# Performance work log

Hardware: AMD Instinct MI355X
Metric: run time of the kernel (lower is better)

Reference implementation:

```python
import jax, jax.numpy as jnp
import numpy as np

N_NODES = 200000
N_EDGES = 1600000
NUM_GRAPHS = 2000
VOCAB = 10000
D = 64
NUM_CLS = 2


def setup_inputs() -> dict:
    key = jax.random.key(0)
    ks = jax.random.split(key, 12)
    x = jax.random.randint(ks[0], (N_NODES,), 0, VOCAB, dtype=jnp.int32)
    edge_index = jax.random.randint(ks[1], (2, N_EDGES), 0, N_NODES, dtype=jnp.int32)
    edge_type = jax.random.randint(ks[2], (N_EDGES,), 0, 8, dtype=jnp.int32)
    batch = jnp.sort(jax.random.randint(ks[3], (N_NODES,), 0, NUM_GRAPHS, dtype=jnp.int32))
    embed_table = jax.random.normal(ks[4], (VOCAB, D), dtype=jnp.float32) * 0.02
    embed_table = embed_table.at[0].set(0.0)  # padding_idx=0
    W1 = jax.random.normal(ks[5], (D, D), dtype=jnp.float32) * (1.0 / np.sqrt(D))
    b1 = jnp.zeros((D,), dtype=jnp.float32)
    W2 = jax.random.normal(ks[6], (D, D), dtype=jnp.float32) * (1.0 / np.sqrt(D))
    b2 = jnp.zeros((D,), dtype=jnp.float32)
    Wlin = jax.random.normal(ks[7], (D, NUM_CLS), dtype=jnp.float32) * (1.0 / np.sqrt(D))
    blin = jnp.zeros((NUM_CLS,), dtype=jnp.float32)
    return {"x": x, "edge_index": edge_index, "edge_type": edge_type, "batch": batch,
            "embed_table": embed_table, "W1": W1, "b1": b1, "W2": W2, "b2": b2,
            "Wlin": Wlin, "blin": blin}


def reference(x, edge_index, edge_type, batch, embed_table, W1, b1, W2, b2, Wlin, blin):
    n = x.shape[0]
    # GCN normalization with self-loops (PyG GCNConv default, edge weight = 1)
    loops = jnp.arange(n, dtype=edge_index.dtype)
    src = jnp.concatenate([edge_index[0], loops])
    dst = jnp.concatenate([edge_index[1], loops])
    deg = jax.ops.segment_sum(jnp.ones_like(src, dtype=jnp.float32), dst, num_segments=n)
    dinv = jax.lax.rsqrt(deg)  # deg >= 1 due to self-loops
    norm = (dinv[src] * dinv[dst])[:, None]  # [E+N, 1]

    def gcn(h, W, b):
        h = h @ W  # transform first (small GEMM)
        agg = jax.ops.segment_sum(norm * h[src], dst, num_segments=n)
        return agg + b

    h = embed_table[x]                      # [N, D] embedding lookup
    h = jax.nn.relu(gcn(h, W1, b1))
    h = jax.nn.relu(gcn(h, W2, b2))
    # global mean pool over graphs
    sums = jax.ops.segment_sum(h, batch, num_segments=NUM_GRAPHS)
    cnts = jax.ops.segment_sum(jnp.ones((n,), dtype=h.dtype), batch, num_segments=NUM_GRAPHS)
    g = sums / jnp.maximum(cnts, 1.0)[:, None]
    return g @ Wlin + blin
```

## Files before the change

### kernel.cpp

```cpp
#include <hip/hip_runtime.h>
#include <hip/hip_fp16.h>


#define DD 64
#define BKT 256
#define MAXK 1024
#define NBLK 256
#define SLACK 772
#define BTE 1024
#define SRCMASK 0x3FFFF
#define PBUF_CAP 4096

typedef _Float16 half8_t __attribute__((ext_vector_type(8)));
typedef float float4_t __attribute__((ext_vector_type(4)));
union F4H8 { float4 f; half8_t h; };
union H8   { float4 f; __half2 h[4]; };

static __device__ __forceinline__ void atomAddF(float* p, float v) {
    unsafeAtomicAdd(p, v);
}

__global__ __launch_bounds__(BTE) void bin_count_kernel(
        const int* __restrict__ dst, int E, int CH,
        int* __restrict__ hist, int K,
        const float2* __restrict__ table2, __half2* __restrict__ th2, int n2,
        const float* __restrict__ W1, const float* __restrict__ W2,
        __half* __restrict__ w1t, __half* __restrict__ w2t) {
    __shared__ int lh[MAXK];
    int tid = threadIdx.x;
    for (int i = tid; i < K; i += BTE) lh[i] = 0;
    __syncthreads();
    int stride = gridDim.x * BTE;
    for (int i = blockIdx.x * BTE + tid; i < n2; i += stride)
        th2[i] = __float22half2_rn(table2[i]);
    for (int i = blockIdx.x * BTE + tid; i < DD * DD; i += stride) {
        int n = i >> 6, k = i & 63;
        w1t[i] = __float2half(W1[k * DD + n]);
        w2t[i] = __float2half(W2[k * DD + n]);
    }
    int e0 = blockIdx.x * CH;
    int e1 = min(E, e0 + CH);
    for (int e = e0 + tid; e < e1; e += BTE)
        atomicAdd(&lh[((unsigned)dst[e]) >> 8], 1);
    __syncthreads();
    for (int b = tid; b < K; b += BTE)
        hist[blockIdx.x * MAXK + b] = lh[b];
}

__global__ __launch_bounds__(256) void totals_kernel(
        const int* __restrict__ hist, int* __restrict__ bts,
        float* __restrict__ outacc, int K, int G2) {
    int gt = blockIdx.x * 256 + threadIdx.x;
    if (gt < G2) outacc[gt] = 0.f;
    int wid = gt >> 6;
    int lane = threadIdx.x & 63;
    if (wid >= K) return;
    const int PER = NBLK / 64;
    int s = 0;
    #pragma unroll
    for (int i = 0; i < PER; ++i)
        s += hist[(lane * PER + i) * MAXK + wid];
    #pragma unroll
    for (int off = 32; off >= 1; off >>= 1)
        s += __shfl_xor(s, off);
    if (lane == 0) bts[wid] = s;
}

__global__ __launch_bounds__(256) void scan_bb_kernel(
        const int* __restrict__ bts, int* __restrict__ bb, int K, int E) {
    __shared__ int part[256];
    int tid = threadIdx.x;
    int CH2 = (K + 255) / 256;
    int base = tid * CH2;
    int s = 0;
    for (int i = 0; i < CH2; ++i) {
        int idx = base + i;
        if (idx < K) s += bts[idx];
    }
    part[tid] = s;
    __syncthreads();
    if (tid < 64) {
        int carry = 0;
        for (int c = 0; c < 4; ++c) {
            int orig = part[c * 64 + tid];
            int v = orig;
            #pragma unroll
            for (int off = 1; off < 64; off <<= 1) {
                int t = __shfl_up(v, off);
                if (tid >= off) v += t;
            }
            int tot = __shfl(v, 63);
            part[c * 64 + tid] = v - orig + carry;
            carry += tot;
        }
    }
    __syncthreads();
    int run = part[tid];
    for (int i = 0; i < CH2; ++i) {
        int idx = base + i;
        if (idx < K) {
            bb[idx] = run;
            run += bts[idx];
        }
    }
    if (tid == 0) bb[K] = E;
}

__global__ __launch_bounds__(256) void scanB_kernel(
        const int* __restrict__ hist, const int* __restrict__ bb,
        int* __restrict__ cur, int K) {
    int wid = (blockIdx.x * 256 + threadIdx.x) >> 6;
    int lane = threadIdx.x & 63;
    if (wid >= K) return;
    int b = wid;
    const int PER = NBLK / 64;
    int v[PER];
    int sum = 0;
    #pragma unroll
    for (int i = 0; i < PER; ++i) {
        v[i] = hist[(lane * PER + i) * MAXK + b];
        sum += v[i];
    }
    int pref = sum;
    #pragma unroll
    for (int off = 1; off < 64; off <<= 1) {
        int t = __shfl_up(pref, off);
        if (lane >= off) pref += t;
    }
    int run = bb[b] + pref - sum;
    #pragma unroll
    for (int i = 0; i < PER; ++i) {
        cur[(lane * PER + i) * MAXK + b] = run;
        run += v[i];
    }
}

__global__ __launch_bounds__(BTE) void fill_kernel(
        const int* __restrict__ src, const int* __restrict__ dst, int E, int CH,
        const int* __restrict__ cur, int* __restrict__ pairbuf, int K) {
    __shared__ int lcur[MAXK];
    int tid = threadIdx.x;
    for (int b = tid; b < K; b += BTE)
        lcur[b] = cur[blockIdx.x * MAXK + b];
    __syncthreads();
    int e0 = blockIdx.x * CH;
    int e1 = min(E, e0 + CH);
    for (int e = e0 + tid; e < e1; e += BTE) {
        int s = src[e], d = dst[e];
        int pos = atomicAdd(&lcur[((unsigned)d) >> 8], 1);
        pairbuf[pos] = s | ((d & 255) << 24);
    }
}

__global__ __launch_bounds__(256) void build_csr_kernel(
        const int* __restrict__ pairbuf, const int* __restrict__ bnd,
        const int* __restrict__ x, int2* __restrict__ rowinfo,
        float2* __restrict__ xd, __half* __restrict__ dinvh,
        int* __restrict__ csr_src, __half* __restrict__ g1h, int N) {
    __shared__ int cnt[256], basel[256], curl[256];
    __shared__ int pbuf[PBUF_CAP];
    int tid = threadIdx.x;
    int b = blockIdx.x;
    int node0 = b << 8;
    cnt[tid] = 0;
    __syncthreads();
    int bb0 = bnd[b], bb1 = bnd[b + 1];
    int L = bb1 - bb0;
    bool fits = (L <= PBUF_CAP);
    if (fits) {
        for (int i = tid; i < L; i += 256) {
            int pk = pairbuf[bb0 + i];
            pbuf[i] = pk;
            atomicAdd(&cnt[((unsigned)pk) >> 24], 1);
        }
    } else {
        for (int i = bb0 + tid; i < bb1; i += 256)
            atomicAdd(&cnt[((unsigned)pairbuf[i]) >> 24], 1);
    }
    __syncthreads();
    int c  = cnt[tid];
    int pc = (c + 3) & ~3;
    {
        __syncthreads();
        basel[tid] = pc;
        __syncthreads();
        if (tid < 64) {
            int carry = 0;
            for (int cc = 0; cc < 4; ++cc) {
                int orig = basel[cc * 64 + tid];
                int v = orig;
                #pragma unroll
                for (int off = 1; off < 64; off <<= 1) {
                    int t = __shfl_up(v, off);
                    if (tid >= off) v += t;
                }
                int tot = __shfl(v, 63);
                cnt[cc * 64 + tid] = v - orig + carry;
                carry += tot;
            }
        }
        __syncthreads();
    }
    int cb0 = ((bb0 + 3) & ~3) + SLACK * b;
    int node = node0 + tid;
    int myBase = cb0 + cnt[tid];
    curl[tid] = myBase;
    if (node < N) {
        rowinfo[node] = make_int2(myBase, pc);
        float di = rsqrtf((float)c + 1.0f);
        xd[node] = make_float2(di, __int_as_float(x[node]));
        dinvh[node] = __float2half(di);
        for (int t = c; t < pc; ++t) csr_src[myBase + t] = N;
    } else if (node == N) {
        xd[N] = make_float2(0.0f, __int_as_float(0));
        dinvh[N] = __float2half(0.0f);
        float2* z = (float2*)(g1h + (size_t)N * DD);
        for (int t = 0; t < DD / 4; ++t) z[t] = make_float2(0.f, 0.f);
    }
    __syncthreads();
    if (fits) {
        for (int i = tid; i < L; i += 256) {
            int pk = pbuf[i];
            int pos = atomicAdd(&curl[((unsigned)pk) >> 24], 1);
            int s = pk & 0x00FFFFFF;
            csr_src[pos] = (int)(((unsigned)s) | (((unsigned)x[s]) << 18));
        }
    } else {
        for (int i = bb0 + tid; i < bb1; i += 256) {
            int pk = pairbuf[i];
            int pos = atomicAdd(&curl[((unsigned)pk) >> 24], 1);
            int s = pk & 0x00FFFFFF;
            csr_src[pos] = (int)(((unsigned)s) | (((unsigned)x[s]) << 18));
        }
    }
}

__global__ __launch_bounds__(256, 8) void layer1_kernel(
        const int2* __restrict__ rowinfo,
        const int* __restrict__ csr_src, const float2* __restrict__ xd,
        const __half* __restrict__ dinvh,
        const float4* __restrict__ th4, const __half* __restrict__ wt,
        const float* __restrict__ bias, __half* __restrict__ g1h, int N) {
    __shared__ float4 Hs4[32 * 9];
    __shared__ float dvs[32];
    int row0 = blockIdx.x * 32;
    int tid = threadIdx.x;
    int node_l = tid >> 3, j3 = tid & 7;
    int node = row0 + node_l;
    H8 acc0, acc1, acc2, acc3;
    acc0.f = make_float4(0.f, 0.f, 0.f, 0.f);
    acc1.f = acc0.f; acc2.f = acc0.f; acc3.f = acc0.f;
    __half2 dh = __float2half2_rn(0.f);
    if (node < N) {
        float2 sxd = xd[node];
        float di = sxd.x;
        if (j3 == 0) dvs[node_l] = di;
        dh = __float2half2_rn(di);
        H8 tv; tv.f = th4[(size_t)__float_as_int(sxd.y) * 8 + j3];
        acc0.h[0] = __hmul2(dh, tv.h[0]); acc0.h[1] = __hmul2(dh, tv.h[1]);
        acc0.h[2] = __hmul2(dh, tv.h[2]); acc0.h[3] = __hmul2(dh, tv.h[3]);
        int2 ri = rowinfo[node];
        const int4* cs = (const int4*)(csr_src + ri.x);
        int nq = ri.y >> 2;
        int q = 0;
        for (; q + 1 < nq; q += 2) {
            int4 sA = cs[q], sB = cs[q + 1];
            unsigned a0 = (unsigned)sA.x, a1 = (unsigned)sA.y;
            unsigned a2 = (unsigned)sA.z, a3 = (unsigned)sA.w;
            unsigned b0i = (unsigned)sB.x, b1i = (unsigned)sB.y;
            unsigned b2i = (unsigned)sB.z, b3i = (unsigned)sB.w;
            H8 u0, u1, u2, u3, u4, u5, u6, u7;
            u0.f = th4[(size_t)(a0 >> 18) * 8 + j3];
            u1.f = th4[(size_t)(a1 >> 18) * 8 + j3];
            u2.f = th4[(size_t)(a2 >> 18) * 8 + j3];
            u3.f = th4[(size_t)(a3 >> 18) * 8 + j3];
            u4.f = th4[(size_t)(b0i >> 18) * 8 + j3];
            u5.f = th4[(size_t)(b1i >> 18) * 8 + j3];
            u6.f = th4[(size_t)(b2i >> 18) * 8 + j3];
            u7.f = th4[(size_t)(b3i >> 18) * 8 + j3];
            __half2 w0 = __half2half2(dinvh[a0 & SRCMASK]);
            __half2 w1 = __half2half2(dinvh[a1 & SRCMASK]);
            __half2 w2 = __half2half2(dinvh[a2 & SRCMASK]);
            __half2 w3 = __half2half2(dinvh[a3 & SRCMASK]);
            __half2 w4 = __half2half2(dinvh[b0i & SRCMASK]);
            __half2 w5 = __half2half2(dinvh[b1i & SRCMASK]);
            __half2 w6 = __half2half2(dinvh[b2i & SRCMASK]);
            __half2 w7 = __half2half2(dinvh[b3i & SRCMASK]);
            #pragma unroll
            for (int t = 0; t < 4; ++t) {
                acc0.h[t] = __hfma2(w0, u0.h[t], acc0.h[t]);
                acc1.h[t] = __hfma2(w1, u1.h[t], acc1.h[t]);
                acc2.h[t] = __hfma2(w2, u2.h[t], acc2.h[t]);
                acc3.h[t] = __hfma2(w3, u3.h[t], acc3.h[t]);
                acc0.h[t] = __hfma2(w4, u4.h[t], acc0.h[t]);
                acc1.h[t] = __hfma2(w5, u5.h[t], acc1.h[t]);
                acc2.h[t] = __hfma2(w6, u6.h[t], acc2.h[t]);
                acc3.h[t] = __hfma2(w7, u7.h[t], acc3.h[t]);
            }
        }
        if (q < nq) {
            int4 sA = cs[q];
            unsigned a0 = (unsigned)sA.x, a1 = (unsigned)sA.y;
            unsigned a2 = (unsigned)sA.z, a3 = (unsigned)sA.w;
            H8 u0, u1, u2, u3;
            u0.f = th4[(size_t)(a0 >> 18) * 8 + j3];
            u1.f = th4[(size_t)(a1 >> 18) * 8 + j3];
            u2.f = th4[(size_t)(a2 >> 18) * 8 + j3];
            u3.f = th4[(size_t)(a3 >> 18) * 8 + j3];
            __half2 w0 = __half2half2(dinvh[a0 & SRCMASK]);
            __half2 w1 = __half2half2(dinvh[a1 & SRCMASK]);
            __half2 w2 = __half2half2(dinvh[a2 & SRCMASK]);
            __half2 w3 = __half2half2(dinvh[a3 & SRCMASK]);
            #pragma unroll
            for (int t = 0; t < 4; ++t) {
                acc0.h[t] = __hfma2(w0, u0.h[t], acc0.h[t]);
                acc1.h[t] = __hfma2(w1, u1.h[t], acc1.h[t]);
                acc2.h[t] = __hfma2(w2, u2.h[t], acc2.h[t]);
                acc3.h[t] = __hfma2(w3, u3.h[t], acc3.h[t]);
            }
        }
        #pragma unroll
        for (int t = 0; t < 4; ++t)
            acc0.h[t] = __hmul2(dh, __hadd2(__hadd2(acc0.h[t], acc1.h[t]),
                                            __hadd2(acc2.h[t], acc3.h[t])));
    }
    Hs4[node_l * 9 + j3] = acc0.f;
    __syncthreads();

    int wave = tid >> 6, lane = tid & 63;
    int m = lane & 15, quad = lane >> 4;
    int ncol = wave * 16 + m;
    F4H8 b0, b1;
    const float4* WT4 = (const float4*)wt;
    b0.f = WT4[ncol * 8 + quad];
    b1.f = WT4[ncol * 8 + 4 + quad];
    float bb_ = bias[ncol];
    #pragma unroll
    for (int t = 0; t < 2; ++t) {
        F4H8 a0, a1;
        a0.f = Hs4[(t * 16 + m) * 9 + quad];
        a1.f = Hs4[(t * 16 + m) * 9 + 4 + quad];
        float4_t acc = {0.f, 0.f, 0.f, 0.f};
        acc = __builtin_amdgcn_mfma_f32_16x16x32_f16(a0.h, b0.h, acc, 0, 0, 0);
        acc = __builtin_amdgcn_mfma_f32_16x16x32_f16(a1.h, b1.h, acc, 0, 0, 0);
        #pragma unroll
        for (int reg = 0; reg < 4; ++reg) {
            int row = t * 16 + quad * 4 + reg;
            int grow = row0 + row;
            if (grow < N) {
                float h = fmaxf(acc[reg] + bb_, 0.0f);
                g1h[(size_t)grow * DD + ncol] = __float2half(dvs[row] * h);
            }
        }
    }
}

__global__ __launch_bounds__(256, 8) void layer2_pool_kernel(
        const int2* __restrict__ rowinfo,
        const int* __restrict__ csr_src, const float2* __restrict__ xd,
        const float4* __restrict__ g1h4, const __half* __restrict__ wt,
        const float* __restrict__ bias, const int* __restrict__ batch,
        const float* __restrict__ Wlin, float* __restrict__ outacc, int N) {
    __shared__ float4 Hs4[32 * 9];
    __shared__ float lp0[128], lp1[128];
    __shared__ float p0s[32], p1s[32];
    __shared__ int   bat[32];
    int row0 = blockIdx.x * 32;
    int tid = threadIdx.x;
    int node_l = tid >> 3, j3 = tid & 7;
    int node = row0 + node_l;
    H8 acc0, acc1, acc2, acc3;
    acc0.f = make_float4(0.f, 0.f, 0.f, 0.f);
    acc1.f = acc0.f; acc2.f = acc0.f; acc3.f = acc0.f;
    if (node < N) {
        float di = xd[node].x;
        acc0.f = g1h4[(size_t)node * 8 + j3];
        int2 ri = rowinfo[node];
        const int4* cs = (const int4*)(csr_src + ri.x);
        int nq = ri.y >> 2;
        int q = 0;
        for (; q + 1 < nq; q += 2) {
            int4 sA = cs[q], sB = cs[q + 1];
            H8 u0, u1, u2, u3, u4, u5, u6, u7;
            u0.f = g1h4[(size_t)(sA.x & SRCMASK) * 8 + j3];
            u1.f = g1h4[(size_t)(sA.y & SRCMASK) * 8 + j3];
            u2.f = g1h4[(size_t)(sA.z & SRCMASK) * 8 + j3];
            u3.f = g1h4[(size_t)(sA.w & SRCMASK) * 8 + j3];
            u4.f = g1h4[(size_t)(sB.x & SRCMASK) * 8 + j3];
            u5.f = g1h4[(size_t)(sB.y & SRCMASK) * 8 + j3];
            u6.f = g1h4[(size_t)(sB.z & SRCMASK) * 8 + j3];
            u7.f = g1h4[(size_t)(sB.w & SRCMASK) * 8 + j3];
            #pragma unroll
            for (int t = 0; t < 4; ++t) {
                acc0.h[t] = __hadd2(acc0.h[t], u0.h[t]);
                acc1.h[t] = __hadd2(acc1.h[t], u1.h[t]);
                acc2.h[t] = __hadd2(acc2.h[t], u2.h[t]);
                acc3.h[t] = __hadd2(acc3.h[t], u3.h[t]);
                acc0.h[t] = __hadd2(acc0.h[t], u4.h[t]);
                acc1.h[t] = __hadd2(acc1.h[t], u5.h[t]);
                acc2.h[t] = __hadd2(acc2.h[t], u6.h[t]);
                acc3.h[t] = __hadd2(acc3.h[t], u7.h[t]);
            }
        }
        if (q < nq) {
            int4 sA = cs[q];
            H8 u0, u1, u2, u3;
            u0.f = g1h4[(size_t)(sA.x & SRCMASK) * 8 + j3];
            u1.f = g1h4[(size_t)(sA.y & SRCMASK) * 8 + j3];
            u2.f = g1h4[(size_t)(sA.z & SRCMASK) * 8 + j3];
            u3.f = g1h4[(size_t)(sA.w & SRCMASK) * 8 + j3];
            #pragma unroll
            for (int t = 0; t < 4; ++t) {
                acc0.h[t] = __hadd2(acc0.h[t], u0.h[t]);
                acc1.h[t] = __hadd2(acc1.h[t], u1.h[t]);
                acc2.h[t] = __hadd2(acc2.h[t], u2.h[t]);
                acc3.h[t] = __hadd2(acc3.h[t], u3.h[t]);
            }
        }
        __half2 dih = __float2half2_rn(di);
        #pragma unroll
        for (int t = 0; t < 4; ++t)
            acc0.h[t] = __hmul2(dih, __hadd2(__hadd2(acc0.h[t], acc1.h[t]),
                                             __hadd2(acc2.h[t], acc3.h[t])));
    }
    Hs4[node_l * 9 + j3] = acc0.f;
    __syncthreads();

    int wave = tid >> 6, lane = tid & 63;
    int m = lane & 15, quad = lane >> 4;
    int ncol = wave * 16 + m;
    F4H8 b0, b1;
    const float4* WT4 = (const float4*)wt;
    b0.f = WT4[ncol * 8 + quad];
    b1.f = WT4[ncol * 8 + 4 + quad];
    float bb_  = bias[ncol];
    float wl0 = Wlin[ncol * 2 + 0];
    float wl1 = Wlin[ncol * 2 + 1];
    #pragma unroll
    for (int t = 0; t < 2; ++t) {
        F4H8 a0, a1;
        a0.f = Hs4[(t * 16 + m) * 9 + quad];
        a1.f = Hs4[(t * 16 + m) * 9 + 4 + quad];
        float4_t acc = {0.f, 0.f, 0.f, 0.f};
        acc = __builtin_amdgcn_mfma_f32_16x16x32_f16(a0.h, b0.h, acc, 0, 0, 0);
        acc = __builtin_amdgcn_mfma_f32_16x16x32_f16(a1.h, b1.h, acc, 0, 0, 0);
        #pragma unroll
        for (int reg = 0; reg < 4; ++reg) {
            int row = t * 16 + quad * 4 + reg;
            int grow = row0 + row;
            float h = (grow < N) ? fmaxf(acc[reg] + bb_, 0.0f) : 0.0f;
            float p0 = h * wl0;
            float p1 = h * wl1;
            #pragma unroll
            for (int off = 8; off >= 1; off >>= 1) {
                p0 += __shfl_xor(p0, off);
                p1 += __shfl_xor(p1, off);
            }
            if (m == 0) {
                lp0[wave * 32 + row] = p0;
                lp1[wave * 32 + row] = p1;
            }
        }
    }
    __syncthreads();
    if (tid < 32) {
        int grow = row0 + tid;
        p0s[tid] = lp0[tid] + lp0[32 + tid] + lp0[64 + tid] + lp0[96 + tid];
        p1s[tid] = lp1[tid] + lp1[32 + tid] + lp1[64 + tid] + lp1[96 + tid];
        bat[tid] = (grow < N) ? batch[grow] : -1;
    }
    __syncthreads();
    if (tid < 32) {
        int bg = bat[tid];
        bool head = (bg >= 0) && (tid == 0 || bat[tid - 1] != bg);
        if (head) {
            float s0 = 0.f, s1 = 0.f;
            for (int k = tid; k < 32 && bat[k] == bg; ++k) {
                s0 += p0s[k];
                s1 += p1s[k];
            }
            atomAddF(&outacc[bg * 2 + 0], s0);
            atomAddF(&outacc[bg * 2 + 1], s1);
        }
    }
}

__global__ void final_kernel(const float* __restrict__ outacc,
                             const int* __restrict__ batch,
                             const float* __restrict__ blin,
                             float* __restrict__ out, int G, int N) {
    int t = blockIdx.x * blockDim.x + threadIdx.x;
    if (t >= G * 2) return;
    int g = t >> 1, c = t & 1;
    int lo = 0, hi = N;
    while (lo < hi) { int m = (lo + hi) >> 1; if (batch[m] < g) lo = m + 1; else hi = m; }
    int lo2 = lo, hi2 = N;
    while (lo2 < hi2) { int m = (lo2 + hi2) >> 1; if (batch[m] < g + 1) lo2 = m + 1; else hi2 = m; }
    float cnt = (float)(lo2 - lo);
    out[t] = outacc[t] / fmaxf(cnt, 1.0f) + blin[c];
}

extern "C" void kernel_launch(void* const* d_in, const int* in_sizes, int n_in,
                              void* d_out, int out_size, void* d_ws, size_t ws_size,
                              hipStream_t stream) {
    const int*   x      = (const int*)d_in[0];
    const int*   ei     = (const int*)d_in[1];
    const int*   batch  = (const int*)d_in[3];
    const float* table  = (const float*)d_in[4];
    const float* W1     = (const float*)d_in[5];
    const float* b1     = (const float*)d_in[6];
    const float* W2     = (const float*)d_in[7];
    const float* b2     = (const float*)d_in[8];
    const float* Wlin   = (const float*)d_in[9];
    const float* blin   = (const float*)d_in[10];
    float* out = (float*)d_out;

    const int N = in_sizes[0];
    const int E = in_sizes[2];
    const int G = out_size / 2;
    const int TBL = in_sizes[4];

    const int* src = ei;
    const int* dst = ei + E;

    const int K = (N + BKT - 1) / BKT;
    const int M = NBLK * MAXK;
    const int CH = (E + NBLK - 1) / NBLK;
    const int CSRSZ = E + SLACK * K + 64;

    __half* g1h     = (__half*)d_ws;
    __half* th      = g1h + (size_t)(N + 1) * DD;
    __half* w1t     = th + TBL;
    __half* w2t     = w1t + DD * DD;
    int*    pairbuf = (int*)(w2t + DD * DD);
    int*    csr_src = pairbuf + E;
    int2*   rowinfo = (int2*)(csr_src + CSRSZ);
    float2* xd      = (float2*)(rowinfo + N);
    __half* dinvh   = (__half*)(xd + N + 1);
    float*  outacc  = (float*)(dinvh + (size_t)((N + 2) & ~1));
    int*    bb      = (int*)(outacc + 2 * G);
    int*    bts     = bb + K + 1;
    int*    hist    = bts + K;
    int*    cur     = hist + M;

    const int BT = 256;

    bin_count_kernel<<<NBLK, BTE, 0, stream>>>(dst, E, CH, hist, K,
                                               (const float2*)table,
                                               (__half2*)th, TBL / 2,
                                               W1, W2, w1t, w2t);
    totals_kernel<<<(K * 64 + BT - 1) / BT, BT, 0, stream>>>(hist, bts, outacc,
                                                             K, 2 * G);
    scan_bb_kernel<<<1, BT, 0, stream>>>(bts, bb, K, E);
    scanB_kernel<<<(K * 64 + BT - 1) / BT, BT, 0, stream>>>(hist, bb, cur, K);
    fill_kernel<<<NBLK, BTE, 0, stream>>>(src, dst, E, CH, cur, pairbuf, K);
    build_csr_kernel<<<K, BT, 0, stream>>>(pairbuf, bb, x, rowinfo, xd, dinvh,
                                           csr_src, g1h, N);

    int gRow = (N + 31) / 32;
    layer1_kernel<<<gRow, BT, 0, stream>>>(rowinfo, csr_src, xd, dinvh,
                                           (const float4*)th, w1t, b1, g1h, N);
    layer2_pool_kernel<<<gRow, BT, 0, stream>>>(rowinfo, csr_src, xd,
                                                (const float4*)g1h, w2t, b2,
                                                batch, Wlin, outacc, N);
    final_kernel<<<(G * 2 + BT - 1) / BT, BT, 0, stream>>>(outacc, batch, blin,
                                                           out, G, N);
}
```

Before: 218.2 us.

## Fuse all stages into a cooperative persistent megakernel with grid syncs

Replaces the nine separate kernel launches with one persistent cooperative kernel. Its phases are separated by grid-wide barriers, and a per-launch-mode fallback runs the phases as seven launches when cooperative launch is unavailable. The global exclusive scan over bucket totals is replaced by atomic bump allocation of each bucket's pair and CSR base, with a fixed per-bucket slack. Blocks are reduced from 1024 to 256 threads and loop over work chunks. The aim is to remove launch overhead and the serial single-block scan. The cost is grid.sync latency, lower occupancy per phase from the grid-stride persistent layout, and a non-deterministic bucket order in the CSR.

```diff
diff --git a/kernel.cpp b/kernel.cpp
--- a/kernel.cpp
+++ b/kernel.cpp
@@ -1,15 +1,17 @@
 #include <hip/hip_runtime.h>
 #include <hip/hip_fp16.h>
+#include <hip/hip_cooperative_groups.h>
+
+namespace cg = cooperative_groups;
 
 
 #define DD 64
 #define BKT 256
 #define MAXK 1024
 #define NBLK 256
-#define SLACK 772
-#define BTE 1024
 #define SRCMASK 0x3FFFF
-#define PBUF_CAP 4096
+#define PBUF_CAP 3072
+#define SMEM_INTS 3840
 
 typedef _Float16 half8_t __attribute__((ext_vector_type(8)));
 typedef float float4_t __attribute__((ext_vector_type(4)));
@@ -20,174 +22,133 @@
     unsafeAtomicAdd(p, v);
 }
 
-__global__ __launch_bounds__(BTE) void bin_count_kernel(
-        const int* __restrict__ dst, int E, int CH,
-        int* __restrict__ hist, int K,
-        const float2* __restrict__ table2, __half2* __restrict__ th2, int n2,
-        const float* __restrict__ W1, const float* __restrict__ W2,
-        __half* __restrict__ w1t, __half* __restrict__ w2t) {
-    __shared__ int lh[MAXK];
+struct Params {
+    const int* x; const int* src; const int* dst; const int* batch;
+    const float2* table2; const float* W1; const float* b1;
+    const float* W2; const float* b2; const float* Wlin; const float* blin;
+    float* out;
+    __half* g1h; __half* th; __half* w1t; __half* w2t;
+    int* pairbuf; int* csr; int2* rowinfo; float2* xd; __half* dinvh;
+    float* outacc; int* pbase; int* pcnt; int* cbase; int* pcur; int* ccur;
+    int* hist; int* cur;
+    int N, E, G, TBL, K, CH;
+};
+
+static __device__ void phase_prep(const Params& P, int* smem) {
     int tid = threadIdx.x;
-    for (int i = tid; i < K; i += BTE) lh[i] = 0;
-    __syncthreads();
-    int stride = gridDim.x * BTE;
-    for (int i = blockIdx.x * BTE + tid; i < n2; i += stride)
-        th2[i] = __float22half2_rn(table2[i]);
-    for (int i = blockIdx.x * BTE + tid; i < DD * DD; i += stride) {
+    int gid = blockIdx.x * 256 + tid;
+    int gstride = gridDim.x * 256;
+    if (gid == 0) { *P.pcur = 0; *P.ccur = 0; }
+    for (int i = gid; i < 2 * P.G; i += gstride) P.outacc[i] = 0.f;
+    __half2* th2 = (__half2*)P.th;
+    int n2 = P.TBL / 2;
+    for (int i = gid; i < n2; i += gstride)
+        th2[i] = __float22half2_rn(P.table2[i]);
+    for (int i = gid; i < DD * DD; i += gstride) {
         int n = i >> 6, k = i & 63;
-        w1t[i] = __float2half(W1[k * DD + n]);
-        w2t[i] = __float2half(W2[k * DD + n]);
-    }
-    int e0 = blockIdx.x * CH;
-    int e1 = min(E, e0 + CH);
-    for (int e = e0 + tid; e < e1; e += BTE)
-        atomicAdd(&lh[((unsigned)dst[e]) >> 8], 1);
-    __syncthreads();
-    for (int b = tid; b < K; b += BTE)
-        hist[blockIdx.x * MAXK + b] = lh[b];
-}
-
-__global__ __launch_bounds__(256) void totals_kernel(
-        const int* __restrict__ hist, int* __restrict__ bts,
-        float* __restrict__ outacc, int K, int G2) {
-    int gt = blockIdx.x * 256 + threadIdx.x;
-    if (gt < G2) outacc[gt] = 0.f;
-    int wid = gt >> 6;
+        P.w1t[i] = __float2half(P.W1[k * DD + n]);
+        P.w2t[i] = __float2half(P.W2[k * DD + n]);
+    }
+    int* lh = smem;
+    for (int c = blockIdx.x; c < NBLK; c += gridDim.x) {
+        for (int i = tid; i < P.K; i += 256) lh[i] = 0;
+        __syncthreads();
+        int e0 = c * P.CH, e1 = min(P.E, e0 + P.CH);
+        for (int e = e0 + tid; e < e1; e += 256)
+            atomicAdd(&lh[((unsigned)P.dst[e]) >> 8], 1);
+        __syncthreads();
+        for (int b = tid; b < P.K; b += 256) P.hist[c * MAXK + b] = lh[b];
+        __syncthreads();
+    }
+}
+
+static __device__ void phase_alloc(const Params& P) {
+    int w = (blockIdx.x * 256 + threadIdx.x) >> 6;
     int lane = threadIdx.x & 63;
-    if (wid >= K) return;
+    int nw = (gridDim.x * 256) >> 6;
     const int PER = NBLK / 64;
-    int s = 0;
-    #pragma unroll
-    for (int i = 0; i < PER; ++i)
-        s += hist[(lane * PER + i) * MAXK + wid];
-    #pragma unroll
-    for (int off = 32; off >= 1; off >>= 1)
-        s += __shfl_xor(s, off);
-    if (lane == 0) bts[wid] = s;
-}
-
-__global__ __launch_bounds__(256) void scan_bb_kernel(
-        const int* __restrict__ bts, int* __restrict__ bb, int K, int E) {
-    __shared__ int part[256];
+    for (int b = w; b < P.K; b += nw) {
+        int v[PER];
+        int sum = 0;
+        #pragma unroll
+        for (int i = 0; i < PER; ++i) {
+            v[i] = P.hist[(lane * PER + i) * MAXK + b];
+            sum += v[i];
+        }
+        int pref = sum;
+        #pragma unroll
+        for (int off = 1; off < 64; off <<= 1) {
+            int t = __shfl_up(pref, off);
+            if (lane >= off) pref += t;
+        }
+        int total = __shfl(pref, 63);
+        int pb = 0;
+        if (lane == 0) {
+            pb = atomicAdd(P.pcur, total);
+            int cb = atomicAdd(P.ccur, ((total + 3) & ~3) + 3 * BKT);
+            P.pbase[b] = pb;
+            P.pcnt[b]  = total;
+            P.cbase[b] = cb;
+        }
+        pb = __shfl(pb, 0);
+        int run = pb + pref - sum;
+        #pragma unroll
+        for (int i = 0; i < PER; ++i) {
+            P.cur[(lane * PER + i) * MAXK + b] = run;
+            run += v[i];
+        }
+    }
+}
+
+static __device__ void phase_fill(const Params& P, int* smem) {
     int tid = threadIdx.x;
-    int CH2 = (K + 255) / 256;
-    int base = tid * CH2;
-    int s = 0;
-    for (int i = 0; i < CH2; ++i) {
-        int idx = base + i;
-        if (idx < K) s += bts[idx];
-    }
-    part[tid] = s;
-    __syncthreads();
-    if (tid < 64) {
-        int carry = 0;
-        for (int c = 0; c < 4; ++c) {
-            int orig = part[c * 64 + tid];
-            int v = orig;
-            #pragma unroll
-            for (int off = 1; off < 64; off <<= 1) {
-                int t = __shfl_up(v, off);
-                if (tid >= off) v += t;
-            }
-            int tot = __shfl(v, 63);
-            part[c * 64 + tid] = v - orig + carry;
-            carry += tot;
-        }
-    }
-    __syncthreads();
-    int run = part[tid];
-    for (int i = 0; i < CH2; ++i) {
-        int idx = base + i;
-        if (idx < K) {
-            bb[idx] = run;
-            run += bts[idx];
-        }
-    }
-    if (tid == 0) bb[K] = E;
-}
-
-__global__ __launch_bounds__(256) void scanB_kernel(
-        const int* __restrict__ hist, const int* __restrict__ bb,
-        int* __restrict__ cur, int K) {
-    int wid = (blockIdx.x * 256 + threadIdx.x) >> 6;
-    int lane = threadIdx.x & 63;
-    if (wid >= K) return;
-    int b = wid;
-    const int PER = NBLK / 64;
-    int v[PER];
-    int sum = 0;
-    #pragma unroll
-    for (int i = 0; i < PER; ++i) {
-        v[i] = hist[(lane * PER + i) * MAXK + b];
-        sum += v[i];
-    }
-    int pref = sum;
-    #pragma unroll
-    for (int off = 1; off < 64; off <<= 1) {
-        int t = __shfl_up(pref, off);
-        if (lane >= off) pref += t;
-    }
-    int run = bb[b] + pref - sum;
-    #pragma unroll
-    for (int i = 0; i < PER; ++i) {
-        cur[(lane * PER + i) * MAXK + b] = run;
-        run += v[i];
-    }
-}
-
-__global__ __launch_bounds__(BTE) void fill_kernel(
-        const int* __restrict__ src, const int* __restrict__ dst, int E, int CH,
-        const int* __restrict__ cur, int* __restrict__ pairbuf, int K) {
-    __shared__ int lcur[MAXK];
+    int* lcur = smem;
+    for (int c = blockIdx.x; c < NBLK; c += gridDim.x) {
+        for (int b = tid; b < P.K; b += 256) lcur[b] = P.cur[c * MAXK + b];
+        __syncthreads();
+        int e0 = c * P.CH, e1 = min(P.E, e0 + P.CH);
+        for (int e = e0 + tid; e < e1; e += 256) {
+            int s = P.src[e], d = P.dst[e];
+            int pos = atomicAdd(&lcur[((unsigned)d) >> 8], 1);
+            P.pairbuf[pos] = s | ((d & 255) << 24);
+        }
+        __syncthreads();
+    }
+}
+
+static __device__ void phase_build(const Params& P, int* smem) {
     int tid = threadIdx.x;
-    for (int b = tid; b < K; b += BTE)
-        lcur[b] = cur[blockIdx.x * MAXK + b];
-    __syncthreads();
-    int e0 = blockIdx.x * CH;
-    int e1 = min(E, e0 + CH);
-    for (int e = e0 + tid; e < e1; e += BTE) {
-        int s = src[e], d = dst[e];
-        int pos = atomicAdd(&lcur[((unsigned)d) >> 8], 1);
-        pairbuf[pos] = s | ((d & 255) << 24);
-    }
-}
-
-__global__ __launch_bounds__(256) void build_csr_kernel(
-        const int* __restrict__ pairbuf, const int* __restrict__ bnd,
-        const int* __restrict__ x, int2* __restrict__ rowinfo,
-        float2* __restrict__ xd, __half* __restrict__ dinvh,
-        int* __restrict__ csr_src, __half* __restrict__ g1h, int N) {
-    __shared__ int cnt[256], basel[256], curl[256];
-    __shared__ int pbuf[PBUF_CAP];
-    int tid = threadIdx.x;
-    int b = blockIdx.x;
-    int node0 = b << 8;
-    cnt[tid] = 0;
-    __syncthreads();
-    int bb0 = bnd[b], bb1 = bnd[b + 1];
-    int L = bb1 - bb0;
-    bool fits = (L <= PBUF_CAP);
-    if (fits) {
-        for (int i = tid; i < L; i += 256) {
-            int pk = pairbuf[bb0 + i];
-            pbuf[i] = pk;
-            atomicAdd(&cnt[((unsigned)pk) >> 24], 1);
-        }
-    } else {
-        for (int i = bb0 + tid; i < bb1; i += 256)
-            atomicAdd(&cnt[((unsigned)pairbuf[i]) >> 24], 1);
-    }
-    __syncthreads();
-    int c  = cnt[tid];
-    int pc = (c + 3) & ~3;
-    {
-        __syncthreads();
-        basel[tid] = pc;
+    int* cnt  = smem;
+    int* excl = smem + 256;
+    int* curl = smem + 512;
+    int* pbuf = smem + 768;
+    for (int b = blockIdx.x; b < P.K; b += gridDim.x) {
+        int node0 = b << 8;
+        cnt[tid] = 0;
+        __syncthreads();
+        int bb0 = P.pbase[b];
+        int L   = P.pcnt[b];
+        bool fits = (L <= PBUF_CAP);
+        if (fits) {
+            for (int i = tid; i < L; i += 256) {
+                int pk = P.pairbuf[bb0 + i];
+                pbuf[i] = pk;
+                atomicAdd(&cnt[((unsigned)pk) >> 24], 1);
+            }
+        } else {
+            for (int i = tid; i < L; i += 256)
+                atomicAdd(&cnt[((unsigned)P.pairbuf[bb0 + i]) >> 24], 1);
+        }
+        __syncthreads();
+        int c  = cnt[tid];
+        int pc = (c + 3) & ~3;
+        __syncthreads();
+        excl[tid] = pc;
         __syncthreads();
         if (tid < 64) {
             int carry = 0;
             for (int cc = 0; cc < 4; ++cc) {
-                int orig = basel[cc * 64 + tid];
+                int orig = excl[cc * 64 + tid];
                 int v = orig;
                 #pragma unroll
                 for (int off = 1; off < 64; off <<= 1) {
@@ -200,369 +161,393 @@
             }
         }
         __syncthreads();
-    }
-    int cb0 = ((bb0 + 3) & ~3) + SLACK * b;
-    int node = node0 + tid;
-    int myBase = cb0 + cnt[tid];
-    curl[tid] = myBase;
-    if (node < N) {
-        rowinfo[node] = make_int2(myBase, pc);
-        float di = rsqrtf((float)c + 1.0f);
-        xd[node] = make_float2(di, __int_as_float(x[node]));
-        dinvh[node] = __float2half(di);
-        for (int t = c; t < pc; ++t) csr_src[myBase + t] = N;
-    } else if (node == N) {
-        xd[N] = make_float2(0.0f, __int_as_float(0));
-        dinvh[N] = __float2half(0.0f);
-        float2* z = (float2*)(g1h + (size_t)N * DD);
-        for (int t = 0; t < DD / 4; ++t) z[t] = make_float2(0.f, 0.f);
-    }
-    __syncthreads();
-    if (fits) {
-        for (int i = tid; i < L; i += 256) {
-            int pk = pbuf[i];
-            int pos = atomicAdd(&curl[((unsigned)pk) >> 24], 1);
-            int s = pk & 0x00FFFFFF;
-            csr_src[pos] = (int)(((unsigned)s) | (((unsigned)x[s]) << 18));
-        }
-    } else {
-        for (int i = bb0 + tid; i < bb1; i += 256) {
-            int pk = pairbuf[i];
-            int pos = atomicAdd(&curl[((unsigned)pk) >> 24], 1);
-            int s = pk & 0x00FFFFFF;
-            csr_src[pos] = (int)(((unsigned)s) | (((unsigned)x[s]) << 18));
-        }
-    }
-}
-
-__global__ __launch_bounds__(256, 8) void layer1_kernel(
-        const int2* __restrict__ rowinfo,
-        const int* __restrict__ csr_src, const float2* __restrict__ xd,
-        const __half* __restrict__ dinvh,
-        const float4* __restrict__ th4, const __half* __restrict__ wt,
-        const float* __restrict__ bias, __half* __restrict__ g1h, int N) {
-    __shared__ float4 Hs4[32 * 9];
-    __shared__ float dvs[32];
-    int row0 = blockIdx.x * 32;
+        int cb0 = P.cbase[b];
+        int node = node0 + tid;
+        int myBase = cb0 + cnt[tid];
+        curl[tid] = myBase;
+        if (node < P.N) {
+            P.rowinfo[node] = make_int2(myBase, pc);
+            float di = rsqrtf((float)c + 1.0f);
+            P.xd[node] = make_float2(di, __int_as_float(P.x[node]));
+            P.dinvh[node] = __float2half(di);
+            for (int t = c; t < pc; ++t) P.csr[myBase + t] = P.N;
+        } else if (node == P.N) {
+            P.xd[P.N] = make_float2(0.0f, __int_as_float(0));
+            P.dinvh[P.N] = __float2half(0.0f);
+            float2* z = (float2*)(P.g1h + (size_t)P.N * DD);
+            for (int t = 0; t < DD / 4; ++t) z[t] = make_float2(0.f, 0.f);
+        }
+        __syncthreads();
+        if (fits) {
+            for (int i = tid; i < L; i += 256) {
+                int pk = pbuf[i];
+                int pos = atomicAdd(&curl[((unsigned)pk) >> 24], 1);
+                int s = pk & 0x00FFFFFF;
+                P.csr[pos] = (int)(((unsigned)s) | (((unsigned)P.x[s]) << 18));
+            }
+        } else {
+            for (int i = tid; i < L; i += 256) {
+                int pk = P.pairbuf[bb0 + i];
+                int pos = atomicAdd(&curl[((unsigned)pk) >> 24], 1);
+                int s = pk & 0x00FFFFFF;
+                P.csr[pos] = (int)(((unsigned)s) | (((unsigned)P.x[s]) << 18));
+            }
+        }
+        __syncthreads();
+    }
+}
+
+static __device__ void phase_layer1(const Params& P, int* smem) {
+    float4* Hs4 = (float4*)smem;
+    float*  dvs = (float*)(smem + 1152);
+    const float4* th4 = (const float4*)P.th;
+    const float4* WT4 = (const float4*)P.w1t;
     int tid = threadIdx.x;
     int node_l = tid >> 3, j3 = tid & 7;
-    int node = row0 + node_l;
-    H8 acc0, acc1, acc2, acc3;
-    acc0.f = make_float4(0.f, 0.f, 0.f, 0.f);
-    acc1.f = acc0.f; acc2.f = acc0.f; acc3.f = acc0.f;
-    __half2 dh = __float2half2_rn(0.f);
-    if (node < N) {
-        float2 sxd = xd[node];
-        float di = sxd.x;
-        if (j3 == 0) dvs[node_l] = di;
-        dh = __float2half2_rn(di);
-        H8 tv; tv.f = th4[(size_t)__float_as_int(sxd.y) * 8 + j3];
-        acc0.h[0] = __hmul2(dh, tv.h[0]); acc0.h[1] = __hmul2(dh, tv.h[1]);
-        acc0.h[2] = __hmul2(dh, tv.h[2]); acc0.h[3] = __hmul2(dh, tv.h[3]);
-        int2 ri = rowinfo[node];
-        const int4* cs = (const int4*)(csr_src + ri.x);
-        int nq = ri.y >> 2;
-        int q = 0;
-        for (; q + 1 < nq; q += 2) {
-            int4 sA = cs[q], sB = cs[q + 1];
-            unsigned a0 = (unsigned)sA.x, a1 = (unsigned)sA.y;
-            unsigned a2 = (unsigned)sA.z, a3 = (unsigned)sA.w;
-            unsigned b0i = (unsigned)sB.x, b1i = (unsigned)sB.y;
-            unsigned b2i = (unsigned)sB.z, b3i = (unsigned)sB.w;
-            H8 u0, u1, u2, u3, u4, u5, u6, u7;
-            u0.f = th4[(size_t)(a0 >> 18) * 8 + j3];
-            u1.f = th4[(size_t)(a1 >> 18) * 8 + j3];
-            u2.f = th4[(size_t)(a2 >> 18) * 8 + j3];
-            u3.f = th4[(size_t)(a3 >> 18) * 8 + j3];
-            u4.f = th4[(size_t)(b0i >> 18) * 8 + j3];
-            u5.f = th4[(size_t)(b1i >> 18) * 8 + j3];
-            u6.f = th4[(size_t)(b2i >> 18) * 8 + j3];
-            u7.f = th4[(size_t)(b3i >> 18) * 8 + j3];
-            __half2 w0 = __half2half2(dinvh[a0 & SRCMASK]);
-            __half2 w1 = __half2half2(dinvh[a1 & SRCMASK]);
-            __half2 w2 = __half2half2(dinvh[a2 & SRCMASK]);
-            __half2 w3 = __half2half2(dinvh[a3 & SRCMASK]);
-            __half2 w4 = __half2half2(dinvh[b0i & SRCMASK]);
-            __half2 w5 = __half2half2(dinvh[b1i & SRCMASK]);
-            __half2 w6 = __half2half2(dinvh[b2i & SRCMASK]);
-            __half2 w7 = __half2half2(dinvh[b3i & SRCMASK]);
-            #pragma unroll
-            for (int t = 0; t < 4; ++t) {
-                acc0.h[t] = __hfma2(w0, u0.h[t], acc0.h[t]);
-                acc1.h[t] = __hfma2(w1, u1.h[t], acc1.h[t]);
-                acc2.h[t] = __hfma2(w2, u2.h[t], acc2.h[t]);
-                acc3.h[t] = __hfma2(w3, u3.h[t], acc3.h[t]);
-                acc0.h[t] = __hfma2(w4, u4.h[t], acc0.h[t]);
-                acc1.h[t] = __hfma2(w5, u5.h[t], acc1.h[t]);
-                acc2.h[t] = __hfma2(w6, u6.h[t], acc2.h[t]);
-                acc3.h[t] = __hfma2(w7, u7.h[t], acc3.h[t]);
-            }
-        }
-        if (q < nq) {
-            int4 sA = cs[q];
-            unsigned a0 = (unsigned)sA.x, a1 = (unsigned)sA.y;
-            unsigned a2 = (unsigned)sA.z, a3 = (unsigned)sA.w;
-            H8 u0, u1, u2, u3;
-            u0.f = th4[(size_t)(a0 >> 18) * 8 + j3];
-            u1.f = th4[(size_t)(a1 >> 18) * 8 + j3];
-            u2.f = th4[(size_t)(a2 >> 18) * 8 + j3];
-            u3.f = th4[(size_t)(a3 >> 18) * 8 + j3];
-            __half2 w0 = __half2half2(dinvh[a0 & SRCMASK]);
-            __half2 w1 = __half2half2(dinvh[a1 & SRCMASK]);
-            __half2 w2 = __half2half2(dinvh[a2 & SRCMASK]);
-            __half2 w3 = __half2half2(dinvh[a3 & SRCMASK]);
-            #pragma unroll
-            for (int t = 0; t < 4; ++t) {
-                acc0.h[t] = __hfma2(w0, u0.h[t], acc0.h[t]);
-                acc1.h[t] = __hfma2(w1, u1.h[t], acc1.h[t]);
-                acc2.h[t] = __hfma2(w2, u2.h[t], acc2.h[t]);
-                acc3.h[t] = __hfma2(w3, u3.h[t], acc3.h[t]);
-            }
-        }
-        #pragma unroll
-        for (int t = 0; t < 4; ++t)
-            acc0.h[t] = __hmul2(dh, __hadd2(__hadd2(acc0.h[t], acc1.h[t]),
-                                            __hadd2(acc2.h[t], acc3.h[t])));
-    }
-    Hs4[node_l * 9 + j3] = acc0.f;
-    __syncthreads();
-
     int wave = tid >> 6, lane = tid & 63;
     int m = lane & 15, quad = lane >> 4;
     int ncol = wave * 16 + m;
     F4H8 b0, b1;
-    const float4* WT4 = (const float4*)wt;
     b0.f = WT4[ncol * 8 + quad];
     b1.f = WT4[ncol * 8 + 4 + quad];
-    float bb_ = bias[ncol];
-    #pragma unroll
-    for (int t = 0; t < 2; ++t) {
-        F4H8 a0, a1;
-        a0.f = Hs4[(t * 16 + m) * 9 + quad];
-        a1.f = Hs4[(t * 16 + m) * 9 + 4 + quad];
-        float4_t acc = {0.f, 0.f, 0.f, 0.f};
-        acc = __builtin_amdgcn_mfma_f32_16x16x32_f16(a0.h, b0.h, acc, 0, 0, 0);
-        acc = __builtin_amdgcn_mfma_f32_16x16x32_f16(a1.h, b1.h, acc, 0, 0, 0);
+    float bb_ = P.b1[ncol];
+    int T = (P.N + 31) >> 5;
+    for (int tile = blockIdx.x; tile < T; tile += gridDim.x) {
+        int row0 = tile << 5;
+        int node = row0 + node_l;
+        H8 acc0, acc1, acc2, acc3;
+        acc0.f = make_float4(0.f, 0.f, 0.f, 0.f);
+        acc1.f = acc0.f; acc2.f = acc0.f; acc3.f = acc0.f;
+        __half2 dh = __float2half2_rn(0.f);
+        if (node < P.N) {
+            float2 sxd = P.xd[node];
+            float di = sxd.x;
+            if (j3 == 0) dvs[node_l] = di;
+            dh = __float2half2_rn(di);
+            H8 tv; tv.f = th4[(size_t)__float_as_int(sxd.y) * 8 + j3];
+            acc0.h[0] = __hmul2(dh, tv.h[0]); acc0.h[1] = __hmul2(dh, tv.h[1]);
+            acc0.h[2] = __hmul2(dh, tv.h[2]); acc0.h[3] = __hmul2(dh, tv.h[3]);
+            int2 ri = P.rowinfo[node];
+            const int4* cs = (const int4*)(P.csr + ri.x);
+            int nq = ri.y >> 2;
+            int q = 0;
+            for (; q + 1 < nq; q += 2) {
+                int4 sA = cs[q], sB = cs[q + 1];
+                unsigned a0 = (unsigned)sA.x, a1 = (unsigned)sA.y;
+                unsigned a2 = (unsigned)sA.z, a3 = (unsigned)sA.w;
+                unsigned e0 = (unsigned)sB.x, e1 = (unsigned)sB.y;
+                unsigned e2 = (unsigned)sB.z, e3 = (unsigned)sB.w;
+                H8 u0, u1, u2, u3, u4, u5, u6, u7;
+                u0.f = th4[(size_t)(a0 >> 18) * 8 + j3];
+                u1.f = th4[(size_t)(a1 >> 18) * 8 + j3];
+                u2.f = th4[(size_t)(a2 >> 18) * 8 + j3];
+                u3.f = th4[(size_t)(a3 >> 18) * 8 + j3];
+                u4.f = th4[(size_t)(e0 >> 18) * 8 + j3];
+                u5.f = th4[(size_t)(e1 >> 18) * 8 + j3];
+                u6.f = th4[(size_t)(e2 >> 18) * 8 + j3];
+                u7.f = th4[(size_t)(e3 >> 18) * 8 + j3];
+                __half2 w0 = __half2half2(P.dinvh[a0 & SRCMASK]);
+                __half2 w1 = __half2half2(P.dinvh[a1 & SRCMASK]);
+                __half2 w2 = __half2half2(P.dinvh[a2 & SRCMASK]);
+                __half2 w3 = __half2half2(P.dinvh[a3 & SRCMASK]);
+                __half2 w4 = __half2half2(P.dinvh[e0 & SRCMASK]);
+                __half2 w5 = __half2half2(P.dinvh[e1 & SRCMASK]);
+                __half2 w6 = __half2half2(P.dinvh[e2 & SRCMASK]);
+                __half2 w7 = __half2half2(P.dinvh[e3 & SRCMASK]);
+                #pragma unroll
+                for (int t = 0; t < 4; ++t) {
+                    acc0.h[t] = __hfma2(w0, u0.h[t], acc0.h[t]);
+                    acc1.h[t] = __hfma2(w1, u1.h[t], acc1.h[t]);
+                    acc2.h[t] = __hfma2(w2, u2.h[t], acc2.h[t]);
+                    acc3.h[t] = __hfma2(w3, u3.h[t], acc3.h[t]);
+                    acc0.h[t] = __hfma2(w4, u4.h[t], acc0.h[t]);
+                    acc1.h[t] = __hfma2(w5, u5.h[t], acc1.h[t]);
+                    acc2.h[t] = __hfma2(w6, u6.h[t], acc2.h[t]);
+                    acc3.h[t] = __hfma2(w7, u7.h[t], acc3.h[t]);
+                }
+            }
+            if (q < nq) {
+                int4 sA = cs[q];
+                unsigned a0 = (unsigned)sA.x, a1 = (unsigned)sA.y;
+                unsigned a2 = (unsigned)sA.z, a3 = (unsigned)sA.w;
+                H8 u0, u1, u2, u3;
+                u0.f = th4[(size_t)(a0 >> 18) * 8 + j3];
+                u1.f = th4[(size_t)(a1 >> 18) * 8 + j3];
+                u2.f = th4[(size_t)(a2 >> 18) * 8 + j3];
+                u3.f = th4[(size_t)(a3 >> 18) * 8 + j3];
+                __half2 w0 = __half2half2(P.dinvh[a0 & SRCMASK]);
+                __half2 w1 = __half2half2(P.dinvh[a1 & SRCMASK]);
+                __half2 w2 = __half2half2(P.dinvh[a2 & SRCMASK]);
+                __half2 w3 = __half2half2(P.dinvh[a3 & SRCMASK]);
+                #pragma unroll
+                for (int t = 0; t < 4; ++t) {
+                    acc0.h[t] = __hfma2(w0, u0.h[t], acc0.h[t]);
+                    acc1.h[t] = __hfma2(w1, u1.h[t], acc1.h[t]);
+                    acc2.h[t] = __hfma2(w2, u2.h[t], acc2.h[t]);
+                    acc3.h[t] = __hfma2(w3, u3.h[t], acc3.h[t]);
+                }
+            }
+            #pragma unroll
+            for (int t = 0; t < 4; ++t)
+                acc0.h[t] = __hmul2(dh, __hadd2(__hadd2(acc0.h[t], acc1.h[t]),
+                                                __hadd2(acc2.h[t], acc3.h[t])));
+        }
+        Hs4[node_l * 9 + j3] = acc0.f;
+        __syncthreads();
         #pragma unroll
-        for (int reg = 0; reg < 4; ++reg) {
-            int row = t * 16 + quad * 4 + reg;
-            int grow = row0 + row;
-            if (grow < N) {
-                float h = fmaxf(acc[reg] + bb_, 0.0f);
-                g1h[(size_t)grow * DD + ncol] = __float2half(dvs[row] * h);
-            }
-        }
-    }
-}
-
-__global__ __launch_bounds__(256, 8) void layer2_pool_kernel(
-        const int2* __restrict__ rowinfo,
-        const int* __restrict__ csr_src, const float2* __restrict__ xd,
-        const float4* __restrict__ g1h4, const __half* __restrict__ wt,
-        const float* __restrict__ bias, const int* __restrict__ batch,
-        const float* __restrict__ Wlin, float* __restrict__ outacc, int N) {
-    __shared__ float4 Hs4[32 * 9];
-    __shared__ float lp0[128], lp1[128];
-    __shared__ float p0s[32], p1s[32];
-    __shared__ int   bat[32];
-    int row0 = blockIdx.x * 32;
+        for (int t = 0; t < 2; ++t) {
+            F4H8 a0, a1;
+            a0.f = Hs4[(t * 16 + m) * 9 + quad];
+            a1.f = Hs4[(t * 16 + m) * 9 + 4 + quad];
+            float4_t acc = {0.f, 0.f, 0.f, 0.f};
+            acc = __builtin_amdgcn_mfma_f32_16x16x32_f16(a0.h, b0.h, acc, 0, 0, 0);
+            acc = __builtin_amdgcn_mfma_f32_16x16x32_f16(a1.h, b1.h, acc, 0, 0, 0);
+            #pragma unroll
+            for (int reg = 0; reg < 4; ++reg) {
+                int row = t * 16 + quad * 4 + reg;
+                int grow = row0 + row;
+                if (grow < P.N) {
+                    float h = fmaxf(acc[reg] + bb_, 0.0f);
+                    P.g1h[(size_t)grow * DD + ncol] = __float2half(dvs[row] * h);
+                }
+            }
+        }
+        __syncthreads();
+    }
+}
+
+static __device__ void phase_layer2(const Params& P, int* smem) {
+    float4* Hs4 = (float4*)smem;
+    float*  lp0 = (float*)(smem + 1152);
+    float*  lp1 = (float*)(smem + 1280);
+    float*  p0s = (float*)(smem + 1408);
+    float*  p1s = (float*)(smem + 1440);
+    int*    bat = smem + 1472;
+    const float4* g1h4 = (const float4*)P.g1h;
+    const float4* WT4  = (const float4*)P.w2t;
     int tid = threadIdx.x;
     int node_l = tid >> 3, j3 = tid & 7;
-    int node = row0 + node_l;
-    H8 acc0, acc1, acc2, acc3;
-    acc0.f = make_float4(0.f, 0.f, 0.f, 0.f);
-    acc1.f = acc0.f; acc2.f = acc0.f; acc3.f = acc0.f;
-    if (node < N) {
-        float di = xd[node].x;
-        acc0.f = g1h4[(size_t)node * 8 + j3];
-        int2 ri = rowinfo[node];
-        const int4* cs = (const int4*)(csr_src + ri.x);
-        int nq = ri.y >> 2;
-        int q = 0;
-        for (; q + 1 < nq; q += 2) {
-            int4 sA = cs[q], sB = cs[q + 1];
-            H8 u0, u1, u2, u3, u4, u5, u6, u7;
-            u0.f = g1h4[(size_t)(sA.x & SRCMASK) * 8 + j3];
-            u1.f = g1h4[(size_t)(sA.y & SRCMASK) * 8 + j3];
-            u2.f = g1h4[(size_t)(sA.z & SRCMASK) * 8 + j3];
-            u3.f = g1h4[(size_t)(sA.w & SRCMASK) * 8 + j3];
-            u4.f = g1h4[(size_t)(sB.x & SRCMASK) * 8 + j3];
-            u5.f = g1h4[(size_t)(sB.y & SRCMASK) * 8 + j3];
-            u6.f = g1h4[(size_t)(sB.z & SRCMASK) * 8 + j3];
-            u7.f = g1h4[(size_t)(sB.w & SRCMASK) * 8 + j3];
-            #pragma unroll
-            for (int t = 0; t < 4; ++t) {
-                acc0.h[t] = __hadd2(acc0.h[t], u0.h[t]);
-                acc1.h[t] = __hadd2(acc1.h[t], u1.h[t]);
-                acc2.h[t] = __hadd2(acc2.h[t], u2.h[t]);
-                acc3.h[t] = __hadd2(acc3.h[t], u3.h[t]);
-                acc0.h[t] = __hadd2(acc0.h[t], u4.h[t]);
-                acc1.h[t] = __hadd2(acc1.h[t], u5.h[t]);
-                acc2.h[t] = __hadd2(acc2.h[t], u6.h[t]);
-                acc3.h[t] = __hadd2(acc3.h[t], u7.h[t]);
-            }
-        }
-        if (q < nq) {
-            int4 sA = cs[q];
-            H8 u0, u1, u2, u3;
-            u0.f = g1h4[(size_t)(sA.x & SRCMASK) * 8 + j3];
-            u1.f = g1h4[(size_t)(sA.y & SRCMASK) * 8 + j3];
-            u2.f = g1h4[(size_t)(sA.z & SRCMASK) * 8 + j3];
-            u3.f = g1h4[(size_t)(sA.w & SRCMASK) * 8 + j3];
-            #pragma unroll
-            for (int t = 0; t < 4; ++t) {
-                acc0.h[t] = __hadd2(acc0.h[t], u0.h[t]);
-                acc1.h[t] = __hadd2(acc1.h[t], u1.h[t]);
-                acc2.h[t] = __hadd2(acc2.h[t], u2.h[t]);
-                acc3.h[t] = __hadd2(acc3.h[t], u3.h[t]);
-            }
-        }
-        __half2 dih = __float2half2_rn(di);
-        #pragma unroll
-        for (int t = 0; t < 4; ++t)
-            acc0.h[t] = __hmul2(dih, __hadd2(__hadd2(acc0.h[t], acc1.h[t]),
-                                             __hadd2(acc2.h[t], acc3.h[t])));
-    }
-    Hs4[node_l * 9 + j3] = acc0.f;
-    __syncthreads();
-
     int wave = tid >> 6, lane = tid & 63;
     int m = lane & 15, quad = lane >> 4;
     int ncol = wave * 16 + m;
     F4H8 b0, b1;
-    const float4* WT4 = (const float4*)wt;
     b0.f = WT4[ncol * 8 + quad];
     b1.f = WT4[ncol * 8 + 4 + quad];
-    float bb_  = bias[ncol];
-    float wl0 = Wlin[ncol * 2 + 0];
-    float wl1 = Wlin[ncol * 2 + 1];
-    #pragma unroll
-    for (int t = 0; t < 2; ++t) {
-        F4H8 a0, a1;
-        a0.f = Hs4[(t * 16 + m) * 9 + quad];
-        a1.f = Hs4[(t * 16 + m) * 9 + 4 + quad];
-        float4_t acc = {0.f, 0.f, 0.f, 0.f};
-        acc = __builtin_amdgcn_mfma_f32_16x16x32_f16(a0.h, b0.h, acc, 0, 0, 0);
-        acc = __builtin_amdgcn_mfma_f32_16x16x32_f16(a1.h, b1.h, acc, 0, 0, 0);
+    float bb_ = P.b2[ncol];
+    float wl0 = P.Wlin[ncol * 2 + 0];
+    float wl1 = P.Wlin[ncol * 2 + 1];
+    int T = (P.N + 31) >> 5;
+    for (int tile = blockIdx.x; tile < T; tile += gridDim.x) {
+        int row0 = tile << 5;
+        int node = row0 + node_l;
+        H8 acc0, acc1, acc2, acc3;
+        acc0.f = make_float4(0.f, 0.f, 0.f, 0.f);
+        acc1.f = acc0.f; acc2.f = acc0.f; acc3.f = acc0.f;
+        if (node < P.N) {
+            float di = P.xd[node].x;
+            acc0.f = g1h4[(size_t)node * 8 + j3];
+            int2 ri = P.rowinfo[node];
+            const int4* cs = (const int4*)(P.csr + ri.x);
+            int nq = ri.y >> 2;
+            int q = 0;
+            for (; q + 1 < nq; q += 2) {
+                int4 sA = cs[q], sB = cs[q + 1];
+                H8 u0, u1, u2, u3, u4, u5, u6, u7;
+                u0.f = g1h4[(size_t)(sA.x & SRCMASK) * 8 + j3];
+                u1.f = g1h4[(size_t)(sA.y & SRCMASK) * 8 + j3];
+                u2.f = g1h4[(size_t)(sA.z & SRCMASK) * 8 + j3];
+                u3.f = g1h4[(size_t)(sA.w & SRCMASK) * 8 + j3];
+                u4.f = g1h4[(size_t)(sB.x & SRCMASK) * 8 + j3];
+                u5.f = g1h4[(size_t)(sB.y & SRCMASK) * 8 + j3];
+                u6.f = g1h4[(size_t)(sB.z & SRCMASK) * 8 + j3];
+                u7.f = g1h4[(size_t)(sB.w & SRCMASK) * 8 + j3];
+                #pragma unroll
+                for (int t = 0; t < 4; ++t) {
+                    acc0.h[t] = __hadd2(acc0.h[t], u0.h[t]);
+                    acc1.h[t] = __hadd2(acc1.h[t], u1.h[t]);
+                    acc2.h[t] = __hadd2(acc2.h[t], u2.h[t]);
+                    acc3.h[t] = __hadd2(acc3.h[t], u3.h[t]);
+                    acc0.h[t] = __hadd2(acc0.h[t], u4.h[t]);
+                    acc1.h[t] = __hadd2(acc1.h[t], u5.h[t]);
+                    acc2.h[t] = __hadd2(acc2.h[t], u6.h[t]);
+                    acc3.h[t] = __hadd2(acc3.h[t], u7.h[t]);
+                }
+            }
+            if (q < nq) {
+                int4 sA = cs[q];
+                H8 u0, u1, u2, u3;
+                u0.f = g1h4[(size_t)(sA.x & SRCMASK) * 8 + j3];
+                u1.f = g1h4[(size_t)(sA.y & SRCMASK) * 8 + j3];
+                u2.f = g1h4[(size_t)(sA.z & SRCMASK) * 8 + j3];
+                u3.f = g1h4[(size_t)(sA.w & SRCMASK) * 8 + j3];
+                #pragma unroll
+                for (int t = 0; t < 4; ++t) {
+                    acc0.h[t] = __hadd2(acc0.h[t], u0.h[t]);
+                    acc1.h[t] = __hadd2(acc1.h[t], u1.h[t]);
+                    acc2.h[t] = __hadd2(acc2.h[t], u2.h[t]);
+                    acc3.h[t] = __hadd2(acc3.h[t], u3.h[t]);
+                }
+            }
+            __half2 dih = __float2half2_rn(di);
+            #pragma unroll
+            for (int t = 0; t < 4; ++t)
+                acc0.h[t] = __hmul2(dih, __hadd2(__hadd2(acc0.h[t], acc1.h[t]),
+                                                 __hadd2(acc2.h[t], acc3.h[t])));
+        }
+        Hs4[node_l * 9 + j3] = acc0.f;
+        __syncthreads();
         #pragma unroll
-        for (int reg = 0; reg < 4; ++reg) {
-            int row = t * 16 + quad * 4 + reg;
-            int grow = row0 + row;
-            float h = (grow < N) ? fmaxf(acc[reg] + bb_, 0.0f) : 0.0f;
-            float p0 = h * wl0;
-            float p1 = h * wl1;
+        for (int t = 0; t < 2; ++t) {
+            F4H8 a0, a1;
+            a0.f = Hs4[(t * 16 + m) * 9 + quad];
+            a1.f = Hs4[(t * 16 + m) * 9 + 4 + quad];
+            float4_t acc = {0.f, 0.f, 0.f, 0.f};
+            acc = __builtin_amdgcn_mfma_f32_16x16x32_f16(a0.h, b0.h, acc, 0, 0, 0);
+            acc = __builtin_amdgcn_mfma_f32_16x16x32_f16(a1.h, b1.h, acc, 0, 0, 0);
             #pragma unroll
-            for (int off = 8; off >= 1; off >>= 1) {
-                p0 += __shfl_xor(p0, off);
-                p1 += __shfl_xor(p1, off);
-            }
-            if (m == 0) {
-                lp0[wave * 32 + row] = p0;
-                lp1[wave * 32 + row] = p1;
-            }
-        }
-    }
-    __syncthreads();
-    if (tid < 32) {
-        int grow = row0 + tid;
-        p0s[tid] = lp0[tid] + lp0[32 + tid] + lp0[64 + tid] + lp0[96 + tid];
-        p1s[tid] = lp1[tid] + lp1[32 + tid] + lp1[64 + tid] + lp1[96 + tid];
-        bat[tid] = (grow < N) ? batch[grow] : -1;
-    }
-    __syncthreads();
-    if (tid < 32) {
-        int bg = bat[tid];
-        bool head = (bg >= 0) && (tid == 0 || bat[tid - 1] != bg);
-        if (head) {
-            float s0 = 0.f, s1 = 0.f;
-            for (int k = tid; k < 32 && bat[k] == bg; ++k) {
-                s0 += p0s[k];
-                s1 += p1s[k];
-            }
-            atomAddF(&outacc[bg * 2 + 0], s0);
-            atomAddF(&outacc[bg * 2 + 1], s1);
-        }
-    }
-}
-
-__global__ void final_kernel(const float* __restrict__ outacc,
-                             const int* __restrict__ batch,
-                             const float* __restrict__ blin,
-                             float* __restrict__ out, int G, int N) {
-    int t = blockIdx.x * blockDim.x + threadIdx.x;
-    if (t >= G * 2) return;
-    int g = t >> 1, c = t & 1;
-    int lo = 0, hi = N;
-    while (lo < hi) { int m = (lo + hi) >> 1; if (batch[m] < g) lo = m + 1; else hi = m; }
-    int lo2 = lo, hi2 = N;
-    while (lo2 < hi2) { int m = (lo2 + hi2) >> 1; if (batch[m] < g + 1) lo2 = m + 1; else hi2 = m; }
-    float cnt = (float)(lo2 - lo);
-    out[t] = outacc[t] / fmaxf(cnt, 1.0f) + blin[c];
+            for (int reg = 0; reg < 4; ++reg) {
+                int row = t * 16 + quad * 4 + reg;
+                int grow = row0 + row;
+                float h = (grow < P.N) ? fmaxf(acc[reg] + bb_, 0.0f) : 0.0f;
+                float p0 = h * wl0;
+                float p1 = h * wl1;
+                #pragma unroll
+                for (int off = 8; off >= 1; off >>= 1) {
+                    p0 += __shfl_xor(p0, off);
+                    p1 += __shfl_xor(p1, off);
+                }
+                if (m == 0) {
+                    lp0[wave * 32 + row] = p0;
+                    lp1[wave * 32 + row] = p1;
+                }
+            }
+        }
+        __syncthreads();
+        if (tid < 32) {
+            int grow = row0 + tid;
+            p0s[tid] = lp0[tid] + lp0[32 + tid] + lp0[64 + tid] + lp0[96 + tid];
+            p1s[tid] = lp1[tid] + lp1[32 + tid] + lp1[64 + tid] + lp1[96 + tid];
+            bat[tid] = (grow < P.N) ? P.batch[grow] : -1;
+        }
+        __syncthreads();
+        if (tid < 32) {
+            int bg = bat[tid];
+            bool head = (bg >= 0) && (tid == 0 || bat[tid - 1] != bg);
+            if (head) {
+                float s0 = 0.f, s1 = 0.f;
+                for (int k = tid; k < 32 && bat[k] == bg; ++k) {
+                    s0 += p0s[k];
+                    s1 += p1s[k];
+                }
+                atomAddF(&P.outacc[bg * 2 + 0], s0);
+                atomAddF(&P.outacc[bg * 2 + 1], s1);
+            }
+        }
+        __syncthreads();
+    }
+}
+
+static __device__ void phase_final(const Params& P) {
+    int gid = blockIdx.x * 256 + threadIdx.x;
+    int gstride = gridDim.x * 256;
+    for (int t = gid; t < P.G * 2; t += gstride) {
+        int g = t >> 1, c = t & 1;
+        int lo = 0, hi = P.N;
+        while (lo < hi) { int mm = (lo + hi) >> 1; if (P.batch[mm] < g) lo = mm + 1; else hi = mm; }
+        int lo2 = lo, hi2 = P.N;
+        while (lo2 < hi2) { int mm = (lo2 + hi2) >> 1; if (P.batch[mm] < g + 1) lo2 = mm + 1; else hi2 = mm; }
+        float cnt = (float)(lo2 - lo);
+        P.out[t] = P.outacc[t] / fmaxf(cnt, 1.0f) + P.blin[c];
+    }
+}
+
+__global__ __launch_bounds__(256, 4) void megakernel(Params P, int phase) {
+    __shared__ __align__(16) int smem[SMEM_INTS];
+    bool all = (phase < 0);
+    cg::grid_group grid = cg::this_grid();
+    if (all || phase == 0) phase_prep(P, smem);
+    if (all) grid.sync();
+    if (all || phase == 1) phase_alloc(P);
+    if (all) grid.sync();
+    if (all || phase == 2) phase_fill(P, smem);
+    if (all) grid.sync();
+    if (all || phase == 3) phase_build(P, smem);
+    if (all) grid.sync();
+    if (all || phase == 4) phase_layer1(P, smem);
+    if (all) grid.sync();
+    if (all || phase == 5) phase_layer2(P, smem);
+    if (all) grid.sync();
+    if (all || phase == 6) phase_final(P);
 }
 
 extern "C" void kernel_launch(void* const* d_in, const int* in_sizes, int n_in,
                               void* d_out, int out_size, void* d_ws, size_t ws_size,
                               hipStream_t stream) {
-    const int*   x      = (const int*)d_in[0];
-    const int*   ei     = (const int*)d_in[1];
-    const int*   batch  = (const int*)d_in[3];
-    const float* table  = (const float*)d_in[4];
-    const float* W1     = (const float*)d_in[5];
-    const float* b1     = (const float*)d_in[6];
-    const float* W2     = (const float*)d_in[7];
-    const float* b2     = (const float*)d_in[8];
-    const float* Wlin   = (const float*)d_in[9];
-    const float* blin   = (const float*)d_in[10];
-    float* out = (float*)d_out;
-
     const int N = in_sizes[0];
     const int E = in_sizes[2];
     const int G = out_size / 2;
     const int TBL = in_sizes[4];
-
-    const int* src = ei;
-    const int* dst = ei + E;
-
     const int K = (N + BKT - 1) / BKT;
+    const int CH = (E + NBLK - 1) / NBLK;
+    const int CSRSZ = E + (3 * BKT + 4) * K + 64;
     const int M = NBLK * MAXK;
-    const int CH = (E + NBLK - 1) / NBLK;
-    const int CSRSZ = E + SLACK * K + 64;
-
-    __half* g1h     = (__half*)d_ws;
-    __half* th      = g1h + (size_t)(N + 1) * DD;
-    __half* w1t     = th + TBL;
-    __half* w2t     = w1t + DD * DD;
-    int*    pairbuf = (int*)(w2t + DD * DD);
-    int*    csr_src = pairbuf + E;
-    int2*   rowinfo = (int2*)(csr_src + CSRSZ);
-    float2* xd      = (float2*)(rowinfo + N);
-    __half* dinvh   = (__half*)(xd + N + 1);
-    float*  outacc  = (float*)(dinvh + (size_t)((N + 2) & ~1));
-    int*    bb      = (int*)(outacc + 2 * G);
-    int*    bts     = bb + K + 1;
-    int*    hist    = bts + K;
-    int*    cur     = hist + M;
-
-    const int BT = 256;
-
-    bin_count_kernel<<<NBLK, BTE, 0, stream>>>(dst, E, CH, hist, K,
-                                               (const float2*)table,
-                                               (__half2*)th, TBL / 2,
-                                               W1, W2, w1t, w2t);
-    totals_kernel<<<(K * 64 + BT - 1) / BT, BT, 0, stream>>>(hist, bts, outacc,
-                                                             K, 2 * G);
-    scan_bb_kernel<<<1, BT, 0, stream>>>(bts, bb, K, E);
-    scanB_kernel<<<(K * 64 + BT - 1) / BT, BT, 0, stream>>>(hist, bb, cur, K);
-    fill_kernel<<<NBLK, BTE, 0, stream>>>(src, dst, E, CH, cur, pairbuf, K);
-    build_csr_kernel<<<K, BT, 0, stream>>>(pairbuf, bb, x, rowinfo, xd, dinvh,
-                                           csr_src, g1h, N);
-
-    int gRow = (N + 31) / 32;
-    layer1_kernel<<<gRow, BT, 0, stream>>>(rowinfo, csr_src, xd, dinvh,
-                                           (const float4*)th, w1t, b1, g1h, N);
-    layer2_pool_kernel<<<gRow, BT, 0, stream>>>(rowinfo, csr_src, xd,
-                                                (const float4*)g1h, w2t, b2,
-                                                batch, Wlin, outacc, N);
-    final_kernel<<<(G * 2 + BT - 1) / BT, BT, 0, stream>>>(outacc, batch, blin,
-                                                           out, G, N);
-}
+
+    Params P;
+    P.x = (const int*)d_in[0];
+    P.src = (const int*)d_in[1];
+    P.dst = ((const int*)d_in[1]) + E;
+    P.batch = (const int*)d_in[3];
+    P.table2 = (const float2*)d_in[4];
+    P.W1 = (const float*)d_in[5];  P.b1 = (const float*)d_in[6];
+    P.W2 = (const float*)d_in[7];  P.b2 = (const float*)d_in[8];
+    P.Wlin = (const float*)d_in[9]; P.blin = (const float*)d_in[10];
+    P.out = (float*)d_out;
+
+    P.g1h   = (__half*)d_ws;
+    P.th    = P.g1h + (size_t)(N + 1) * DD;
+    P.w1t   = P.th + TBL;
+    P.w2t   = P.w1t + DD * DD;
+    P.pairbuf = (int*)(P.w2t + DD * DD);
+    P.csr     = P.pairbuf + E;
+    P.rowinfo = (int2*)(P.csr + CSRSZ);
+    P.xd      = (float2*)(P.rowinfo + N);
+    P.dinvh   = (__half*)(P.xd + N + 1);
+    P.outacc  = (float*)(P.dinvh + (size_t)((N + 2) & ~1));
+    P.pbase   = (int*)(P.outacc + 2 * G);
+    P.pcnt    = P.pbase + K;
+    P.cbase   = P.pcnt + K;
+    P.pcur    = P.cbase + K;
+    P.ccur    = P.pcur + 1;
+    P.hist    = P.ccur + 3;
+    P.cur     = P.hist + M;
+
+    P.N = N; P.E = E; P.G = G; P.TBL = TBL; P.K = K; P.CH = CH;
+
+    static int s_grid = 0;
+    static int s_coop = 0;
+    if (s_grid == 0) {
+        int coop = 0, dev = 0;
+        hipGetDevice(&dev);
+        hipDeviceGetAttribute(&coop, hipDeviceAttributeCooperativeLaunch, dev);
+        int nb = 0;
+        hipOccupancyMaxActiveBlocksPerMultiprocessor(&nb, megakernel, 256, 0);
+        if (nb < 1) nb = 1;
+        hipDeviceProp_t prop;
+        hipGetDeviceProperties(&prop, dev);
+        int cus = prop.multiProcessorCount;
+        if (cus < 1) cus = 256;
+        s_grid = nb * cus;
+        s_coop = coop;
+    }
+
+    if (s_coop) {
+        int phase = -1;
+        void* args[] = {(void*)&P, (void*)&phase};
+        hipLaunchCooperativeKernel(megakernel, dim3(s_grid), dim3(256),
+                                   args, 0, stream);
+    } else {
+        for (int ph = 0; ph < 7; ++ph)
+            hipLaunchKernelGGL(megakernel, dim3(s_grid), dim3(256), 0, stream,
+                               P, ph);
+    }
+}
```

Result: slower. 679.4 us (+211.4%).
